# Performance work log

Measured on AMD Instinct MI355X. Metric: run time of the kernel, lower is better.

Reference implementation:

```python
import jax, jax.numpy as jnp
import numpy as np

EPS = 1e-3  # BatchNorm eps (eval mode: running_mean=0, running_var=1)
GRID_D, GRID_H, GRID_W, GRID_C = 10, 400, 352, 128


def bn_last(x, g, b):
    # BatchNorm1d eval over last (channel) axis
    return x * (g / jnp.sqrt(1.0 + EPS)) + b


def bn_ch(x, g, b):
    # BatchNorm3d eval, channel axis 1 of NCDHW
    s = (g / jnp.sqrt(1.0 + EPS)).reshape(1, -1, 1, 1, 1)
    return x * s + b.reshape(1, -1, 1, 1, 1)


def vfe_layer(x, W, g, b):
    # x: [N, T, Cin] -> [N, T, 2*units]
    h = jnp.einsum('ntc,uc->ntu', x, W)
    h = jax.nn.relu(bn_last(h, g, b))
    agg = jnp.max(h, axis=1, keepdims=True)          # [N,1,units]
    return jnp.concatenate([h, jnp.broadcast_to(agg, h.shape)], axis=2)


def pad3(x, p):
    # torch ConstantPad3d order: (Wl, Wr, Hl, Hr, Dl, Dr); x is NCDHW
    return jnp.pad(x, ((0, 0), (0, 0), (p[4], p[5]), (p[2], p[3]), (p[0], p[1])))


def conv3d(x, w, stride):
    return jax.lax.conv_general_dilated(
        x, w, window_strides=stride, padding='VALID',
        dimension_numbers=('NCDHW', 'OIDHW', 'NCDHW'))


def setup_inputs() -> dict:
    key = jax.random.key(0)
    ks = jax.random.split(key, 12)
    N, T = 20000, 35
    features = jax.random.normal(ks[0], (N, T, 4), jnp.float32)
    num_voxels = jax.random.randint(ks[1], (N,), 1, T + 1, jnp.int32)
    cb = jnp.zeros((N, 1), jnp.int32)
    cd = jax.random.randint(ks[2], (N, 1), 0, GRID_D, jnp.int32)
    ch = jax.random.randint(ks[3], (N, 1), 0, GRID_H, jnp.int32)
    cw = jax.random.randint(ks[4], (N, 1), 0, GRID_W, jnp.int32)
    coors = jnp.concatenate([cb, cd, ch, cw], axis=1)

    def lin(k, o, i):
        return jax.random.normal(k, (o, i), jnp.float32) / np.sqrt(i)

    def cw3(k, o, i):
        return jax.random.normal(k, (o, i, 3, 3, 3), jnp.float32) / np.sqrt(i * 27)

    return {
        'features': features, 'num_voxels': num_voxels, 'coors': coors, 'batch_size': 1,
        'w_vfe1': lin(ks[5], 16, 7), 'g_vfe1': jnp.ones(16), 'b_vfe1': jnp.zeros(16),
        'w_vfe2': lin(ks[6], 64, 32), 'g_vfe2': jnp.ones(64), 'b_vfe2': jnp.zeros(64),
        'w_lin': lin(ks[7], 128, 128), 'g_lin': jnp.ones(128), 'b_lin': jnp.zeros(128),
        'w_c1': cw3(ks[8], 64, 128), 'g_c1': jnp.ones(64), 'b_c1': jnp.zeros(64),
        'w_c2': cw3(ks[9], 64, 64), 'g_c2': jnp.ones(64), 'b_c2': jnp.zeros(64),
        'w_c3': cw3(ks[10], 64, 64), 'g_c3': jnp.ones(64), 'b_c3': jnp.zeros(64),
    }


def reference(features, num_voxels, coors, batch_size,
              w_vfe1, g_vfe1, b_vfe1, w_vfe2, g_vfe2, b_vfe2,
              w_lin, g_lin, b_lin,
              w_c1, g_c1, b_c1, w_c2, g_c2, b_c2, w_c3, g_c3, b_c3):
    # --- VoxelFeatureExtractor ---
    nv = num_voxels.astype(features.dtype)[:, None, None]
    points_mean = features[:, :, :3].sum(axis=1, keepdims=True) / nv
    rel = features[:, :, :3] - points_mean
    f = jnp.concatenate([features, rel], axis=-1)                 # [N,T,7]
    T = f.shape[1]
    mask = (jnp.arange(T)[None, :] < num_voxels[:, None]).astype(f.dtype)[..., None]
    x = vfe_layer(f, w_vfe1, g_vfe1, b_vfe1) * mask               # [N,T,32]
    x = vfe_layer(x, w_vfe2, g_vfe2, b_vfe2) * mask               # [N,T,128]
    x = jnp.einsum('ntc,uc->ntu', x, w_lin)
    x = jax.nn.relu(bn_last(x, g_lin, b_lin)) * mask
    voxelwise = jnp.max(x, axis=1)                                # [N,128]

    # --- MiddleExtractor: scatter_nd + 3D convs ---
    grid = jnp.zeros((batch_size, GRID_D, GRID_H, GRID_W, GRID_C), f.dtype)
    grid = grid.at[coors[:, 0], coors[:, 1], coors[:, 2], coors[:, 3]].set(voxelwise)
    r = grid.transpose(0, 4, 1, 2, 3)                             # NCDHW [1,128,10,400,352]
    r = pad3(r, (1, 1, 1, 1, 1, 1))
    r = jax.nn.relu(bn_ch(conv3d(r, w_c1, (2, 1, 1)), g_c1, b_c1))  # [1,64,5,400,352]
    r = pad3(r, (1, 1, 1, 1, 0, 0))
    r = jax.nn.relu(bn_ch(conv3d(r, w_c2, (1, 1, 1)), g_c2, b_c2))  # [1,64,3,400,352]
    r = pad3(r, (1, 1, 1, 1, 1, 1))
    r = jax.nn.relu(bn_ch(conv3d(r, w_c3, (2, 1, 1)), g_c3, b_c3))  # [1,64,2,400,352]
    Nb, C, D, H, W = r.shape
    return r.reshape(Nb, C * D, H, W)                             # [1,128,400,352]
```

## Files before the change

kernel.cpp:

```cpp
#include <hip/hip_runtime.h>
#include <hip/hip_bf16.h>

#define BNC 0.99950037f
#define GH 400
#define GW 352

typedef __bf16 bf16_t;
typedef __bf16 bf16x8 __attribute__((ext_vector_type(8)));
typedef __bf16 bf16x4 __attribute__((ext_vector_type(4)));
typedef float f32x4 __attribute__((ext_vector_type(4)));

__global__ void k_winner(const int* __restrict__ coors, int* __restrict__ winner, int N) {
    int i = blockIdx.x * 256 + threadIdx.x;
    if (i >= N) return;
    int d = coors[i*4+1], h = coors[i*4+2], w = coors[i*4+3];
    atomicMax(&winner[(d*GH + h)*GW + w], i);
}

__global__ void k_tr_w(const float* __restrict__ w, float* __restrict__ wt, int CI, int CO) {
    int idx = blockIdx.x * 256 + threadIdx.x;
    int total = 27 * CI * CO;
    if (idx >= total) return;
    int j   = idx & 3;
    int t1  = idx >> 2;
    int co  = t1 % CO;
    int t2  = t1 / CO;
    int ci4 = t2 % (CI/4);
    int tap = t2 / (CI/4);
    int ci  = ci4*4 + j;
    wt[idx] = w[(co*CI + ci)*27 + tap];
}

__global__ void k_tr_lin(const float* __restrict__ wl, float* __restrict__ WT) {
    int idx = blockIdx.x * 256 + threadIdx.x;
    if (idx >= 16384) return;
    int u = idx & 127, c = idx >> 7;
    WT[c*128 + u] = wl[u*128 + c];
}

__global__ void k_prep(const float* __restrict__ g, const float* __restrict__ b,
                       float* __restrict__ out) {
    int i = threadIdx.x;
    if (i < 64)       out[i] = g[i] * BNC;
    else if (i < 128) out[i] = b[i-64];
}

__global__ void k_packw(const float* __restrict__ w, bf16_t* __restrict__ wh,
                        bf16_t* __restrict__ wlo) {
    int i = blockIdx.x * 256 + threadIdx.x;
    if (i >= 13824) return;
    int lane = i & 63, ct = (i >> 6) & 3, s = i >> 8;
    int tap = s >> 1, h = s & 1;
    int kg = lane >> 4, wl = lane & 15;
    int co = ct*16 + wl;
    #pragma unroll
    for (int j = 0; j < 8; ++j) {
        int ci = h*32 + kg*8 + j;
        float v = w[(co*64 + ci)*27 + tap];
        bf16_t hi = (bf16_t)v;
        wh[(long)i*8 + j]  = hi;
        wlo[(long)i*8 + j] = (bf16_t)(v - (float)hi);
    }
}

__global__ __launch_bounds__(128) void k_vfe(
    const float* __restrict__ feats, const int* __restrict__ nvox,
    const float* __restrict__ w1, const float* __restrict__ g1g, const float* __restrict__ b1g,
    const float* __restrict__ w2g, const float* __restrict__ g2g, const float* __restrict__ b2g,
    const float* __restrict__ WT, const float* __restrict__ glg, const float* __restrict__ blg,
    float* __restrict__ voxelwise)
{
    __shared__ float F[35*8];
    __shared__ float W1s[16*8];
    __shared__ float SG1[16], SB1[16];
    __shared__ float X1[35*20];
    __shared__ float X2[35*68];
    __shared__ float RED[4*128];
    __shared__ float AGG1[16];
    __shared__ float AGG2[64];
    __shared__ float Y2B[64];
    __shared__ float YB[128];
    __shared__ float MEANS[3];

    int tid = threadIdx.x;
    int vox = blockIdx.x;
    int nv  = nvox[vox];

    const float* fsrc = feats + (long)vox * 140;
    for (int idx = tid; idx < 140; idx += 128) { int t = idx>>2, c = idx&3; F[t*8+c] = fsrc[idx]; }
    if (tid < 35) F[tid*8+7] = 0.f;
    if (tid < 112) { int u = tid/7, c = tid - u*7; W1s[u*8+c] = w1[tid]; }
    if (tid < 16)  { W1s[tid*8+7] = 0.f; SG1[tid] = g1g[tid]*BNC; SB1[tid] = b1g[tid]; }
    __syncthreads();

    if (tid < 3) {
        float s = 0.f;
        for (int t = 0; t < 35; ++t) s += F[t*8 + tid];
        MEANS[tid] = s / (float)nv;
    }
    __syncthreads();
    for (int idx = tid; idx < 105; idx += 128) { int t = idx/3, c = idx - t*3; F[t*8+4+c] = F[t*8+c] - MEANS[c]; }
    __syncthreads();

    {
        const float4* Ff4  = (const float4*)F;
        const float4* W1f4 = (const float4*)W1s;
        for (int idx = tid; idx < 560; idx += 128) {
            int t = idx >> 4, u = idx & 15;
            float4 a0 = Ff4[t*2], a1 = Ff4[t*2+1];
            float4 b0 = W1f4[u*2], b1v = W1f4[u*2+1];
            float a = a0.x*b0.x + a0.y*b0.y + a0.z*b0.z + a0.w*b0.w
                    + a1.x*b1v.x + a1.y*b1v.y + a1.z*b1v.z + a1.w*b1v.w;
            X1[t*20+u] = fmaxf(a*SG1[u] + SB1[u], 0.f);
        }
    }
    __syncthreads();
    if (tid < 16) {
        float m = 0.f;
        for (int t = 0; t < 35; ++t) m = fmaxf(m, X1[t*20+tid]);
        AGG1[tid] = m;
    }
    __syncthreads();
    if (tid < 64) {
        const float4* wsrc = (const float4*)(w2g + tid*32 + 16);
        const float4* A1f4 = (const float4*)AGG1;
        float a = 0.f;
        #pragma unroll
        for (int q = 0; q < 4; ++q) {
            float4 w4 = wsrc[q], x4 = A1f4[q];
            a += x4.x*w4.x + x4.y*w4.y + x4.z*w4.z + x4.w*w4.w;
        }
        Y2B[tid] = a;
    }
    __syncthreads();

    {
        int u = tid & 63, tg = tid >> 6;
        float w2r[16];
        const float4* wsrc = (const float4*)(w2g + u*32);
        #pragma unroll
        for (int q = 0; q < 4; ++q) {
            float4 w4 = wsrc[q];
            w2r[q*4] = w4.x; w2r[q*4+1] = w4.y; w2r[q*4+2] = w4.z; w2r[q*4+3] = w4.w;
        }
        float su = g2g[u]*BNC, bu = b2g[u];
        float yb2 = Y2B[u];
        float lm = (nv < 35) ? fmaxf(bu, 0.f) : 0.f;
        for (int t = tg; t < nv; t += 2) {
            const float4* xr = (const float4*)(X1 + t*20);
            float a = yb2;
            #pragma unroll
            for (int q = 0; q < 4; ++q) {
                float4 x4 = xr[q];
                a += x4.x*w2r[q*4] + x4.y*w2r[q*4+1] + x4.z*w2r[q*4+2] + x4.w*w2r[q*4+3];
            }
            float h = fmaxf(a*su + bu, 0.f);
            X2[t*68 + u] = h;
            lm = fmaxf(lm, h);
        }
        RED[tg*64 + u] = lm;
    }
    __syncthreads();
    if (tid < 64) AGG2[tid] = fmaxf(RED[tid], RED[64+tid]);
    __syncthreads();
    {
        float a = 0.f;
        for (int c = 0; c < 64; ++c) a = fmaf(AGG2[c], WT[(64 + c)*128 + tid], a);
        YB[tid] = a;
    }
    __syncthreads();

    {
        int ug = tid & 31, tg4 = tid >> 5;
        int u0 = ug * 4;
        int kmax = (nv > tg4) ? ((nv - tg4 + 3) >> 2) : 0;
        float acc[9][4];
        #pragma unroll
        for (int k = 0; k < 9; ++k)
            #pragma unroll
            for (int j = 0; j < 4; ++j) acc[k][j] = 0.f;

        const float4* X2f4 = (const float4*)X2;
        const float4* WTf4 = (const float4*)WT;
        for (int c4 = 0; c4 < 16; ++c4) {
            float4 wv[4];
            #pragma unroll
            for (int cc = 0; cc < 4; ++cc)
                wv[cc] = WTf4[(c4*4+cc)*32 + ug];
            #pragma unroll
            for (int k = 0; k < 9; ++k) {
                if (k < kmax) {
                    int t = tg4 + (k << 2);
                    float4 x4 = X2f4[t*17 + c4];
                    #pragma unroll
                    for (int cc = 0; cc < 4; ++cc) {
                        float xs = (cc == 0) ? x4.x : (cc == 1) ? x4.y : (cc == 2) ? x4.z : x4.w;
                        acc[k][0] = fmaf(xs, wv[cc].x, acc[k][0]);
                        acc[k][1] = fmaf(xs, wv[cc].y, acc[k][1]);
                        acc[k][2] = fmaf(xs, wv[cc].z, acc[k][2]);
                        acc[k][3] = fmaf(xs, wv[cc].w, acc[k][3]);
                    }
                }
            }
        }
        float4 g0 = *(const float4*)(glg + u0);
        float4 b0 = *(const float4*)(blg + u0);
        float4 y0 = *(const float4*)(YB + u0);
        float sg[4] = {g0.x*BNC, g0.y*BNC, g0.z*BNC, g0.w*BNC};
        float sb[4] = {b0.x, b0.y, b0.z, b0.w};
        float yv[4] = {y0.x, y0.y, y0.z, y0.w};
        float m[4];
        #pragma unroll
        for (int j = 0; j < 4; ++j) m[j] = 0.f;
        #pragma unroll
        for (int k = 0; k < 9; ++k) {
            if (k < kmax) {
                #pragma unroll
                for (int j = 0; j < 4; ++j)
                    m[j] = fmaxf(m[j], fmaxf((acc[k][j] + yv[j])*sg[j] + sb[j], 0.f));
            }
        }
        #pragma unroll
        for (int j = 0; j < 4; ++j) RED[tg4*128 + u0 + j] = m[j];
    }
    __syncthreads();
    {
        float m = RED[tid];
        #pragma unroll
        for (int r = 1; r < 4; ++r) m = fmaxf(m, RED[r*128 + tid]);
        voxelwise[(long)vox*128 + tid] = m;
    }
}

__global__ __launch_bounds__(256) void k_gat1(
    const float4* __restrict__ voxf4, const int* __restrict__ winner,
    const float4* __restrict__ Wt1, bf16_t* __restrict__ accH,
    bf16_t* __restrict__ accL, const float* __restrict__ gact,
    int h_lo, int AR)
{
    int r  = blockIdx.y;
    int oh = h_lo + r;
    if ((unsigned)oh >= (unsigned)GH) return;
    int doo = blockIdx.z;
    int w0  = blockIdx.x * 32;

    __shared__ int sList[306];
    __shared__ int sCnt;
    __shared__ float4 sF[32][32];

    int t = threadIdx.x;
    if (t == 0) sCnt = 0;
    __syncthreads();
    for (int idx = t; idx < 306; idx += 256) {
        int x = idx % 34, q = idx / 34;
        int kd = q / 3, kh = q - kd*3;
        int dp = doo*2 + kd - 1;
        int hp = oh + kh - 1;
        int wp = w0 - 1 + x;
        if ((unsigned)dp < 10u && (unsigned)hp < (unsigned)GH && (unsigned)wp < (unsigned)GW) {
            int v = winner[(dp*GH + hp)*GW + wp];
            if (v >= 0) {
                int p = atomicAdd(&sCnt, 1);
                sList[p] = (v << 10) | (kd << 8) | (kh << 6) | x;
            }
        }
    }
    __syncthreads();
    int cnt = sCnt;

    int co = t & 63, wv = t >> 6;
    int ibase = wv*8;
    float acc[8];
    #pragma unroll
    for (int i = 0; i < 8; ++i) acc[i] = 0.f;

    for (int c0 = 0; c0 < cnt; c0 += 32) {
        int nch = min(32, cnt - c0);
        __syncthreads();
        for (int idx = t; idx < nch*32; idx += 256) {
            int slot = idx >> 5, c = idx & 31;
            int widx = sList[c0 + slot] >> 10;
            sF[slot][c] = voxf4[(long)widx*32 + c];
        }
        __syncthreads();
        for (int e = 0; e < nch; ++e) {
            int ent = sList[c0 + e];
            int x = ent & 63, kh = (ent >> 6) & 3, kd = (ent >> 8) & 3;
            #pragma unroll
            for (int kw = 0; kw < 3; ++kw) {
                int i = x - kw;
                if (i >= ibase && i < ibase + 8) {
                    const float4* wb = Wt1 + (long)(kd*9 + kh*3 + kw)*2048 + co;
                    float a = 0.f;
                    #pragma unroll 4
                    for (int c4 = 0; c4 < 32; ++c4) {
                        float4 wq = wb[c4*64];
                        float4 f4 = sF[e][c4];
                        a += f4.x*wq.x + f4.y*wq.y + f4.z*wq.z + f4.w*wq.w;
                    }
                    int j = i - ibase;
                    #pragma unroll
                    for (int j8 = 0; j8 < 8; ++j8)
                        if (j8 == j) acc[j8] += a;
                }
            }
        }
    }

    float g = gact[co], b = gact[64 + co];
    long rowb = ((long)doo*AR + r)*GW + w0;
    #pragma unroll
    for (int i = 0; i < 8; ++i) {
        float rr = fmaxf(acc[i]*g + b, 0.f);
        bf16_t hi = (bf16_t)rr;
        long idx = (rowb + ibase + i)*64 + co;
        accH[idx] = hi;
        accL[idx] = (bf16_t)(rr - (float)hi);
    }
}

__global__ __launch_bounds__(256) void k_convm(
    const bf16_t* __restrict__ srcH, const bf16_t* __restrict__ srcL,
    int src_h0, long src_dpitch,
    float* __restrict__ dstF, bf16_t* __restrict__ dstH, bf16_t* __restrict__ dstL,
    int dst_h0, long sC, long sD, long sH,
    const bf16_t* __restrict__ wph, const bf16_t* __restrict__ wpl,
    const float* __restrict__ gout, const float* __restrict__ bout,
    int D_in, int d_stride, int d_pad, int y0, int nrows)
{
    int oh0 = y0 + (int)blockIdx.y*2;

    __shared__ __align__(16) char smem[17408];
    bf16_t* sAh = (bf16_t*)smem;
    bf16_t* sAl = (bf16_t*)(smem + 8448);
    float*  sOut = (float*)smem;

    int t = threadIdx.x;
    int lane = t & 63, wv = t >> 6;
    int wl = lane & 15, kg = lane >> 4;
    int mh = wv >> 1, cth = wv & 1;
    int w0 = (int)blockIdx.x * 64;
    int od = (int)blockIdx.z;

    f32x4 acc[2][2][2];
    #pragma unroll
    for (int o = 0; o < 2; ++o)
        #pragma unroll
        for (int a = 0; a < 2; ++a)
            #pragma unroll
            for (int b = 0; b < 2; ++b) acc[o][a][b] = (f32x4){0.f, 0.f, 0.f, 0.f};

    const bf16x8* WH = (const bf16x8*)wph;
    const bf16x8* WL = (const bf16x8*)wpl;

    for (int kd = 0; kd < 3; ++kd) {
        int dp = od*d_stride + kd - d_pad;
        if (dp < 0 || dp >= D_in) continue;
        const bf16_t* sdbH = srcH + dp*src_dpitch;
        const bf16_t* sdbL = srcL + dp*src_dpitch;
        #pragma unroll
        for (int sr = 0; sr < 4; ++sr) {
            int hp = oh0 - 1 + sr;
            bool vh = ((unsigned)hp < (unsigned)GH);
            long rowoff = (long)(hp - src_h0) * (GW*64);
            __syncthreads();
            for (int c = t; c < 1056; c += 256) {
                int pl = (c >= 528) ? 1 : 0;
                int cc = c - (pl << 9) - (pl << 4);
                int g = cc / 66, w = cc - g*66;
                int gw = w0 - 1 + w;
                bf16x8 vvv;
                if (vh && (unsigned)gw < (unsigned)GW) {
                    const bf16_t* plane = pl ? sdbL : sdbH;
                    vvv = *(const bf16x8*)(plane + rowoff + (long)gw*64 + g*8);
                } else {
                    #pragma unroll
                    for (int e = 0; e < 8; ++e) vvv[e] = (bf16_t)0.f;
                }
                bf16_t* dstl = pl ? sAl : sAh;
                *(bf16x8*)&dstl[(g*66 + w)*8] = vvv;
            }
            __syncthreads();
            #pragma unroll
            for (int h = 0; h < 2; ++h) {
                #pragma unroll
                for (int kw = 0; kw < 3; ++kw) {
                    bf16x8 Ah[2], Al[2];
                    #pragma unroll
                    for (int mt = 0; mt < 2; ++mt) {
                        int ai = ((h*4 + kg)*66 + (mh*2 + mt)*16 + kw + wl)*8;
                        Ah[mt] = *(const bf16x8*)&sAh[ai];
                        Al[mt] = *(const bf16x8*)&sAl[ai];
                    }
                    #pragma unroll
                    for (int oi = 0; oi < 2; ++oi) {
                        int kh = sr - oi;
                        if (kh >= 0 && kh < 3) {
                            int s = ((kd*3 + kh)*3 + kw)*2 + h;
                            long fb = (long)(s*4 + cth*2)*64 + lane;
                            bf16x8 B0h = WH[fb],      B0l = WL[fb];
                            bf16x8 B1h = WH[fb + 64], B1l = WL[fb + 64];
                            #pragma unroll
                            for (int mt = 0; mt < 2; ++mt) {
                                acc[oi][mt][0] = __builtin_amdgcn_mfma_f32_16x16x32_bf16(Ah[mt], B0h, acc[oi][mt][0], 0, 0, 0);
                                acc[oi][mt][0] = __builtin_amdgcn_mfma_f32_16x16x32_bf16(Ah[mt], B0l, acc[oi][mt][0], 0, 0, 0);
                                acc[oi][mt][0] = __builtin_amdgcn_mfma_f32_16x16x32_bf16(Al[mt], B0h, acc[oi][mt][0], 0, 0, 0);
                                acc[oi][mt][1] = __builtin_amdgcn_mfma_f32_16x16x32_bf16(Ah[mt], B1h, acc[oi][mt][1], 0, 0, 0);
                                acc[oi][mt][1] = __builtin_amdgcn_mfma_f32_16x16x32_bf16(Ah[mt], B1l, acc[oi][mt][1], 0, 0, 0);
                                acc[oi][mt][1] = __builtin_amdgcn_mfma_f32_16x16x32_bf16(Al[mt], B1h, acc[oi][mt][1], 0, 0, 0);
                            }
                        }
                    }
                }
            }
        }
    }

    float so[2], bo[2];
    #pragma unroll
    for (int ct = 0; ct < 2; ++ct) {
        int co = (cth*2 + ct)*16 + wl;
        so[ct] = gout[co]*BNC; bo[ct] = bout[co];
    }
    if (dstF) {
        #pragma unroll
        for (int oi = 0; oi < 2; ++oi) {
            int oh = oh0 + oi;
            bool rv = ((unsigned)oh < (unsigned)GH) && ((int)blockIdx.y*2 + oi < nrows);
            if (rv) {
                #pragma unroll
                for (int mt = 0; mt < 2; ++mt) {
                    int ow = w0 + (mh*2 + mt)*16 + kg*4;
                    if (ow < GW) {
                        #pragma unroll
                        for (int ct = 0; ct < 2; ++ct) {
                            int co = (cth*2 + ct)*16 + wl;
                            f32x4 r;
                            #pragma unroll
                            for (int e = 0; e < 4; ++e)
                                r[e] = fmaxf(acc[oi][mt][ct][e]*so[ct] + bo[ct], 0.f);
                            *(f32x4*)&dstF[(long)co*sC + (long)od*sD + (long)(oh - dst_h0)*sH + ow] = r;
                        }
                    }
                }
            }
        }
    } else {
        __syncthreads();
        #pragma unroll
        for (int oi = 0; oi < 2; ++oi) {
            int oh = oh0 + oi;
            bool rv = ((unsigned)oh < (unsigned)GH) && ((int)blockIdx.y*2 + oi < nrows);
            if (rv) {
                #pragma unroll
                for (int mt = 0; mt < 2; ++mt)
                    #pragma unroll
                    for (int ct = 0; ct < 2; ++ct) {
                        int co = (cth*2 + ct)*16 + wl;
                        #pragma unroll
                        for (int e = 0; e < 4; ++e) {
                            int owl = (mh*2 + mt)*16 + kg*4 + e;
                            sOut[owl*68 + co] = fmaxf(acc[oi][mt][ct][e]*so[ct] + bo[ct], 0.f);
                        }
                    }
                __syncthreads();
                for (int f = t; f < 1024; f += 256) {
                    int w = f >> 4, c4 = f & 15;
                    if (w0 + w < GW) {
                        float4 v = *(const float4*)&sOut[w*68 + c4*4];
                        long base = (long)od*sD + (long)(oh - dst_h0)*sH + (long)(w0 + w)*64 + c4*4;
                        bf16_t h0 = (bf16_t)v.x, h1 = (bf16_t)v.y, h2 = (bf16_t)v.z, h3 = (bf16_t)v.w;
                        bf16x4 hv; hv[0]=h0; hv[1]=h1; hv[2]=h2; hv[3]=h3;
                        bf16x4 lv;
                        lv[0]=(bf16_t)(v.x-(float)h0); lv[1]=(bf16_t)(v.y-(float)h1);
                        lv[2]=(bf16_t)(v.z-(float)h2); lv[3]=(bf16_t)(v.w-(float)h3);
                        *(bf16x4*)&dstH[base] = hv;
                        *(bf16x4*)&dstL[base] = lv;
                    }
                }
                __syncthreads();
            }
        }
    }
}

extern "C" void kernel_launch(void* const* d_in, const int* in_sizes, int n_in,
                              void* d_out, int out_size, void* d_ws, size_t ws_size,
                              hipStream_t stream)
{
    const float* feats = (const float*)d_in[0];
    const int*   nvox  = (const int*)d_in[1];
    const int*   coors = (const int*)d_in[2];
    const float* w1  = (const float*)d_in[4];
    const float* g1  = (const float*)d_in[5];
    const float* b1  = (const float*)d_in[6];
    const float* w2  = (const float*)d_in[7];
    const float* g2  = (const float*)d_in[8];
    const float* b2  = (const float*)d_in[9];
    const float* wl  = (const float*)d_in[10];
    const float* gl  = (const float*)d_in[11];
    const float* bl  = (const float*)d_in[12];
    const float* wc1 = (const float*)d_in[13];
    const float* gc1 = (const float*)d_in[14];
    const float* bc1 = (const float*)d_in[15];
    const float* wc2 = (const float*)d_in[16];
    const float* gc2 = (const float*)d_in[17];
    const float* bc2 = (const float*)d_in[18];
    const float* wc3 = (const float*)d_in[19];
    const float* gc3 = (const float*)d_in[20];
    const float* bc3 = (const float*)d_in[21];

    int N = in_sizes[1];

    auto al = [](size_t b) { return (b + 255) & ~(size_t)255; };

    size_t winB = al((size_t)10*GH*GW*4);
    size_t voxB = al((size_t)N*128*4);
    size_t w1B  = al((size_t)27*128*64*4);
    size_t wlB  = al((size_t)128*128*4);
    size_t wpB  = al((size_t)13824*8*2);
    int NS = 20;
    const int cand[8] = {1, 2, 4, 5, 8, 10, 16, 20};
    for (int k = 0; k < 8; ++k) {
        int ns = cand[k], sh = 400/ns, ar = sh + 4, xr = sh + 2;
        size_t tot = 2*al((size_t)5*ar*GW*64*2) + 2*al((size_t)3*xr*GW*64*2)
                   + winB + voxB + w1B + wlB + 4*wpB + 4096;
        if (tot + (1<<16) <= ws_size) { NS = ns; break; }
    }
    int SH = 400/NS, AR = SH + 4, XR = SH + 2;

    char* ws = (char*)d_ws;
    size_t off = 0;
    auto alloc = [&](size_t bytes) -> void* {
        void* p = ws + off; off += al(bytes); return p;
    };
    size_t accB = (size_t)5*AR*GW*64*2;
    size_t actB = (size_t)3*XR*GW*64*2;
    bf16_t* accH   = (bf16_t*)alloc(accB);
    bf16_t* accL   = (bf16_t*)alloc(accB);
    bf16_t* actH   = (bf16_t*)alloc(actB);
    bf16_t* actL   = (bf16_t*)alloc(actB);
    int*    winner = (int*)alloc((size_t)10*GH*GW*4);
    float*  voxw   = (float*)alloc((size_t)N*128*4);
    float*  wt1    = (float*)alloc((size_t)27*128*64*4);
    float*  wtl    = (float*)alloc((size_t)128*128*4);
    bf16_t* wp2h   = (bf16_t*)alloc(wpB);
    bf16_t* wp2l   = (bf16_t*)alloc(wpB);
    bf16_t* wp3h   = (bf16_t*)alloc(wpB);
    bf16_t* wp3l   = (bf16_t*)alloc(wpB);
    float*  gact   = (float*)alloc(256*4);

    hipMemsetAsync(winner, 0xFF, (size_t)10*GH*GW*4, stream);

    k_tr_w<<<(27*128*64 + 255)/256, 256, 0, stream>>>(wc1, wt1, 128, 64);
    k_tr_lin<<<64, 256, 0, stream>>>(wl, wtl);
    k_packw<<<54, 256, 0, stream>>>(wc2, wp2h, wp2l);
    k_packw<<<54, 256, 0, stream>>>(wc3, wp3h, wp3l);
    k_prep<<<1, 256, 0, stream>>>(gc1, bc1, gact);

    k_winner<<<(N + 255)/256, 256, 0, stream>>>(coors, winner, N);
    k_vfe<<<N, 128, 0, stream>>>(feats, nvox, w1, g1, b1, w2, g2, b2,
                                 wtl, gl, bl, voxw);

    for (int s = 0; s < NS; ++s) {
        k_gat1<<<dim3(11, AR, 5), 256, 0, stream>>>(
            (const float4*)voxw, winner, (const float4*)wt1,
            accH, accL, gact, s*SH - 2, AR);
        k_convm<<<dim3(6, (SH + 2 + 1)/2, 3), 256, 0, stream>>>(
            accH, accL, s*SH - 2, (long)AR*GW*64,
            nullptr, actH, actL, s*SH - 1, 0L, (long)XR*GW*64, (long)GW*64,
            wp2h, wp2l, gc2, bc2,
            5, 1, 0, s*SH - 1, SH + 2);
        k_convm<<<dim3(6, (SH + 1)/2, 2), 256, 0, stream>>>(
            actH, actL, s*SH - 1, (long)XR*GW*64,
            (float*)d_out, nullptr, nullptr, 0, (long)2*GH*GW, (long)GH*GW, (long)GW,
            wp3h, wp3l, gc3, bc3,
            3, 2, 1, s*SH, SH);
    }
}
```

Before: 1.018 ms.

## Prefetch conv input rows into registers and swizzle blocks across XCDs

The 3D conv kernel now uses a flattened stage loop over valid (kd, row) pairs. The next stage's global loads are issued into registers while the current stage's MFMAs run, so global latency overlaps with compute instead of sitting between two barriers. Per-thread staging addresses are precomputed once. Both the gather and conv kernels switch to 1D grids with an XCD-aware block remap so neighbouring tiles land on the same XCD for L2 reuse. This costs more registers per thread, which may reduce occupancy.

```diff
diff --git a/kernel.cpp b/kernel.cpp
--- a/kernel.cpp
+++ b/kernel.cpp
@@ -9,6 +9,13 @@
 typedef __bf16 bf16x8 __attribute__((ext_vector_type(8)));
 typedef __bf16 bf16x4 __attribute__((ext_vector_type(4)));
 typedef float f32x4 __attribute__((ext_vector_type(4)));
+
+__device__ __forceinline__ int xcd_swz(int orig, int nwg) {
+    int q = nwg >> 3, r = nwg & 7;
+    int xcd = orig & 7;
+    int base = (xcd < r) ? xcd*(q+1) : r*(q+1) + (xcd - r)*q;
+    return base + (orig >> 3);
+}
 
 __global__ void k_winner(const int* __restrict__ coors, int* __restrict__ winner, int N) {
     int i = blockIdx.x * 256 + threadIdx.x;
@@ -238,11 +245,15 @@
     bf16_t* __restrict__ accL, const float* __restrict__ gact,
     int h_lo, int AR)
 {
-    int r  = blockIdx.y;
+    int lg = xcd_swz((int)blockIdx.x, (int)gridDim.x);
+    int bx = lg % 11;
+    int t1a = lg / 11;
+    int r  = t1a % AR;
+    int doo = t1a / AR;
+
     int oh = h_lo + r;
     if ((unsigned)oh >= (unsigned)GH) return;
-    int doo = blockIdx.z;
-    int w0  = blockIdx.x * 32;
+    int w0 = bx * 32;
 
     __shared__ int sList[306];
     __shared__ int sCnt;
@@ -326,9 +337,15 @@
     int dst_h0, long sC, long sD, long sH,
     const bf16_t* __restrict__ wph, const bf16_t* __restrict__ wpl,
     const float* __restrict__ gout, const float* __restrict__ bout,
-    int D_in, int d_stride, int d_pad, int y0, int nrows)
+    int D_in, int d_stride, int d_pad, int y0, int nrows, int ny)
 {
-    int oh0 = y0 + (int)blockIdx.y*2;
+    int lg = xcd_swz((int)blockIdx.x, (int)gridDim.x);
+    int bx = lg % 6;
+    int t1a = lg / 6;
+    int by = t1a % ny;
+    int od = t1a / ny;
+    int oh0 = y0 + by*2;
+    int w0  = bx * 64;
 
     __shared__ __align__(16) char smem[17408];
     bf16_t* sAh = (bf16_t*)smem;
@@ -339,8 +356,25 @@
     int lane = t & 63, wv = t >> 6;
     int wl = lane & 15, kg = lane >> 4;
     int mh = wv >> 1, cth = wv & 1;
-    int w0 = (int)blockIdx.x * 64;
-    int od = (int)blockIdx.z;
+
+    int kdlo = max(0, d_pad - od*d_stride);
+    int kdhi = min(3, D_in + d_pad - od*d_stride);
+    int nst = (kdhi - kdlo) * 4;
+
+    int s_pl[5], s_gw[5], s_cc[5];
+    bool s_in[5];
+    #pragma unroll
+    for (int k = 0; k < 5; ++k) {
+        int c = t + k*256;
+        int cl = (c < 1056) ? c : 0;
+        int pl = (cl >= 528) ? 1 : 0;
+        int cc = cl - pl*528;
+        int g = cc / 66, w = cc - g*66;
+        int gw = w0 - 1 + w;
+        s_pl[k] = pl; s_cc[k] = cc; s_gw[k] = gw*64 + g*8;
+        s_in[k] = ((unsigned)gw < (unsigned)GW);
+    }
+    bool has5 = (t < 32);
 
     f32x4 acc[2][2][2];
     #pragma unroll
@@ -353,62 +387,70 @@
     const bf16x8* WH = (const bf16x8*)wph;
     const bf16x8* WL = (const bf16x8*)wpl;
 
-    for (int kd = 0; kd < 3; ++kd) {
+    bf16x8 pre[5];
+    auto issue = [&](int st) {
+        int kd = kdlo + (st >> 2);
         int dp = od*d_stride + kd - d_pad;
-        if (dp < 0 || dp >= D_in) continue;
-        const bf16_t* sdbH = srcH + dp*src_dpitch;
-        const bf16_t* sdbL = srcL + dp*src_dpitch;
-        #pragma unroll
-        for (int sr = 0; sr < 4; ++sr) {
-            int hp = oh0 - 1 + sr;
-            bool vh = ((unsigned)hp < (unsigned)GH);
-            long rowoff = (long)(hp - src_h0) * (GW*64);
-            __syncthreads();
-            for (int c = t; c < 1056; c += 256) {
-                int pl = (c >= 528) ? 1 : 0;
-                int cc = c - (pl << 9) - (pl << 4);
-                int g = cc / 66, w = cc - g*66;
-                int gw = w0 - 1 + w;
-                bf16x8 vvv;
-                if (vh && (unsigned)gw < (unsigned)GW) {
-                    const bf16_t* plane = pl ? sdbL : sdbH;
-                    vvv = *(const bf16x8*)(plane + rowoff + (long)gw*64 + g*8);
+        int sr = st & 3;
+        int hp = oh0 - 1 + sr;
+        bool vh = ((unsigned)hp < (unsigned)GH);
+        long ro = dp*src_dpitch + (long)(hp - src_h0)*(GW*64);
+        #pragma unroll
+        for (int k = 0; k < 5; ++k) {
+            if (k < 4 || has5) {
+                if (vh && s_in[k]) {
+                    const bf16_t* plane = s_pl[k] ? srcL : srcH;
+                    pre[k] = *(const bf16x8*)(plane + ro + s_gw[k]);
                 } else {
                     #pragma unroll
-                    for (int e = 0; e < 8; ++e) vvv[e] = (bf16_t)0.f;
+                    for (int e = 0; e < 8; ++e) pre[k][e] = (bf16_t)0.f;
                 }
-                bf16_t* dstl = pl ? sAl : sAh;
-                *(bf16x8*)&dstl[(g*66 + w)*8] = vvv;
-            }
-            __syncthreads();
+            }
+        }
+    };
+
+    issue(0);
+    for (int st = 0; st < nst; ++st) {
+        __syncthreads();
+        #pragma unroll
+        for (int k = 0; k < 5; ++k) {
+            if (k < 4 || has5) {
+                bf16_t* dl = s_pl[k] ? sAl : sAh;
+                *(bf16x8*)&dl[s_cc[k]*8] = pre[k];
+            }
+        }
+        if (st + 1 < nst) issue(st + 1);
+        __syncthreads();
+
+        int kd = kdlo + (st >> 2);
+        int sr = st & 3;
+        #pragma unroll
+        for (int h = 0; h < 2; ++h) {
             #pragma unroll
-            for (int h = 0; h < 2; ++h) {
+            for (int kw = 0; kw < 3; ++kw) {
+                bf16x8 Ah[2], Al[2];
                 #pragma unroll
-                for (int kw = 0; kw < 3; ++kw) {
-                    bf16x8 Ah[2], Al[2];
-                    #pragma unroll
-                    for (int mt = 0; mt < 2; ++mt) {
-                        int ai = ((h*4 + kg)*66 + (mh*2 + mt)*16 + kw + wl)*8;
-                        Ah[mt] = *(const bf16x8*)&sAh[ai];
-                        Al[mt] = *(const bf16x8*)&sAl[ai];
-                    }
-                    #pragma unroll
-                    for (int oi = 0; oi < 2; ++oi) {
-                        int kh = sr - oi;
-                        if (kh >= 0 && kh < 3) {
-                            int s = ((kd*3 + kh)*3 + kw)*2 + h;
-                            long fb = (long)(s*4 + cth*2)*64 + lane;
-                            bf16x8 B0h = WH[fb],      B0l = WL[fb];
-                            bf16x8 B1h = WH[fb + 64], B1l = WL[fb + 64];
-                            #pragma unroll
-                            for (int mt = 0; mt < 2; ++mt) {
-                                acc[oi][mt][0] = __builtin_amdgcn_mfma_f32_16x16x32_bf16(Ah[mt], B0h, acc[oi][mt][0], 0, 0, 0);
-                                acc[oi][mt][0] = __builtin_amdgcn_mfma_f32_16x16x32_bf16(Ah[mt], B0l, acc[oi][mt][0], 0, 0, 0);
-                                acc[oi][mt][0] = __builtin_amdgcn_mfma_f32_16x16x32_bf16(Al[mt], B0h, acc[oi][mt][0], 0, 0, 0);
-                                acc[oi][mt][1] = __builtin_amdgcn_mfma_f32_16x16x32_bf16(Ah[mt], B1h, acc[oi][mt][1], 0, 0, 0);
-                                acc[oi][mt][1] = __builtin_amdgcn_mfma_f32_16x16x32_bf16(Ah[mt], B1l, acc[oi][mt][1], 0, 0, 0);
-                                acc[oi][mt][1] = __builtin_amdgcn_mfma_f32_16x16x32_bf16(Al[mt], B1h, acc[oi][mt][1], 0, 0, 0);
-                            }
+                for (int mt = 0; mt < 2; ++mt) {
+                    int ai = ((h*4 + kg)*66 + (mh*2 + mt)*16 + kw + wl)*8;
+                    Ah[mt] = *(const bf16x8*)&sAh[ai];
+                    Al[mt] = *(const bf16x8*)&sAl[ai];
+                }
+                #pragma unroll
+                for (int oi = 0; oi < 2; ++oi) {
+                    int kh = sr - oi;
+                    if ((unsigned)kh < 3u) {
+                        int s = ((kd*3 + kh)*3 + kw)*2 + h;
+                        long fb = (long)(s*4 + cth*2)*64 + lane;
+                        bf16x8 B0h = WH[fb],      B0l = WL[fb];
+                        bf16x8 B1h = WH[fb + 64], B1l = WL[fb + 64];
+                        #pragma unroll
+                        for (int mt = 0; mt < 2; ++mt) {
+                            acc[oi][mt][0] = __builtin_amdgcn_mfma_f32_16x16x32_bf16(Ah[mt], B0h, acc[oi][mt][0], 0, 0, 0);
+                            acc[oi][mt][0] = __builtin_amdgcn_mfma_f32_16x16x32_bf16(Ah[mt], B0l, acc[oi][mt][0], 0, 0, 0);
+                            acc[oi][mt][0] = __builtin_amdgcn_mfma_f32_16x16x32_bf16(Al[mt], B0h, acc[oi][mt][0], 0, 0, 0);
+                            acc[oi][mt][1] = __builtin_amdgcn_mfma_f32_16x16x32_bf16(Ah[mt], B1h, acc[oi][mt][1], 0, 0, 0);
+                            acc[oi][mt][1] = __builtin_amdgcn_mfma_f32_16x16x32_bf16(Ah[mt], B1l, acc[oi][mt][1], 0, 0, 0);
+                            acc[oi][mt][1] = __builtin_amdgcn_mfma_f32_16x16x32_bf16(Al[mt], B1h, acc[oi][mt][1], 0, 0, 0);
                         }
                     }
                 }
@@ -426,7 +468,7 @@
         #pragma unroll
         for (int oi = 0; oi < 2; ++oi) {
             int oh = oh0 + oi;
-            bool rv = ((unsigned)oh < (unsigned)GH) && ((int)blockIdx.y*2 + oi < nrows);
+            bool rv = ((unsigned)oh < (unsigned)GH) && (by*2 + oi < nrows);
             if (rv) {
                 #pragma unroll
                 for (int mt = 0; mt < 2; ++mt) {
@@ -450,7 +492,7 @@
         #pragma unroll
         for (int oi = 0; oi < 2; ++oi) {
             int oh = oh0 + oi;
-            bool rv = ((unsigned)oh < (unsigned)GH) && ((int)blockIdx.y*2 + oi < nrows);
+            bool rv = ((unsigned)oh < (unsigned)GH) && (by*2 + oi < nrows);
             if (rv) {
                 #pragma unroll
                 for (int mt = 0; mt < 2; ++mt)
@@ -563,18 +605,20 @@
                                  wtl, gl, bl, voxw);
 
     for (int s = 0; s < NS; ++s) {
-        k_gat1<<<dim3(11, AR, 5), 256, 0, stream>>>(
+        k_gat1<<<11*AR*5, 256, 0, stream>>>(
             (const float4*)voxw, winner, (const float4*)wt1,
             accH, accL, gact, s*SH - 2, AR);
-        k_convm<<<dim3(6, (SH + 2 + 1)/2, 3), 256, 0, stream>>>(
+        int ny2 = (SH + 2 + 1)/2;
+        k_convm<<<6*ny2*3, 256, 0, stream>>>(
             accH, accL, s*SH - 2, (long)AR*GW*64,
             nullptr, actH, actL, s*SH - 1, 0L, (long)XR*GW*64, (long)GW*64,
             wp2h, wp2l, gc2, bc2,
-            5, 1, 0, s*SH - 1, SH + 2);
-        k_convm<<<dim3(6, (SH + 1)/2, 2), 256, 0, stream>>>(
+            5, 1, 0, s*SH - 1, SH + 2, ny2);
+        int ny3 = (SH + 1)/2;
+        k_convm<<<6*ny3*2, 256, 0, stream>>>(
             actH, actL, s*SH - 1, (long)XR*GW*64,
             (float*)d_out, nullptr, nullptr, 0, (long)2*GH*GW, (long)GH*GW, (long)GW,
             wp3h, wp3l, gc3, bc3,
-            3, 2, 1, s*SH, SH);
-    }
-}
+            3, 2, 1, s*SH, SH, ny3);
+    }
+}
```

After: 1.020 ms. Within noise of the previous version (+0.2%).
